# Kernel optimization log

Measured on AMD Instinct MI355X. Metric: run time of the kernel, lower is better.

Reference implementation:

```python
import jax, jax.numpy as jnp
import numpy as np

N_NODES = 50000
N_EDGES = 1600000
IN_CH = 128
OUT_CH = 16
K_HOPS = 2


def setup_inputs() -> dict:
    key = jax.random.key(0)
    k1, k2, k3, k4 = jax.random.split(key, 4)
    x = jax.random.normal(k1, (N_NODES, IN_CH), dtype=jnp.float32)
    W = jax.random.normal(k2, (OUT_CH, IN_CH), dtype=jnp.float32) * 0.05
    edge_weight = jax.random.uniform(k3, (N_EDGES,), dtype=jnp.float32)
    edge_index = jax.random.randint(k4, (2, N_EDGES), 0, N_NODES, dtype=jnp.int64)
    return {"x": x, "W": W, "edge_weight": edge_weight,
            "edge_index": edge_index, "K": K_HOPS}


def reference(x, W, edge_weight, edge_index, K):
    N = x.shape[0]
    # --- gcn_norm with add_self_loops=True (fill_value = 1.0) ---
    loops = jnp.arange(N, dtype=edge_index.dtype)
    row = jnp.concatenate([edge_index[0], loops])  # source nodes
    col = jnp.concatenate([edge_index[1], loops])  # target nodes
    w = jnp.concatenate([edge_weight, jnp.ones((N,), dtype=x.dtype)])
    deg = jax.ops.segment_sum(w, col, num_segments=N)  # degree at targets
    dinv = jnp.where(deg > 0, jax.lax.rsqrt(deg), 0.0)
    norm = dinv[row] * w * dinv[col]  # [E+N]

    # --- K-hop propagation: h <- A_hat @ h (gather-scale-scatter) ---
    def hop(h, _):
        msgs = norm[:, None] * h[row]               # [E+N, F] gather + scale
        h = jax.ops.segment_sum(msgs, col, num_segments=N)  # scatter-add
        return h, None

    h, _ = jax.lax.scan(hop, x, None, length=K)

    # --- linear projection (bias=False) then log_softmax over classes ---
    logits = h @ W.T  # [N, out_channels]
    return jax.nn.log_softmax(logits, axis=1)
```

## Files before the change

### kernel.cpp

```cpp
#include <hip/hip_runtime.h>
#include <hip/hip_fp16.h>
#include <math.h>

#define IN_CH 128
#define OUT_CH 16
#define B 256
#define CH_H 2048
#define CH_P 4096
#define LSH 6
#define LNODES 64
#define S2 4
#define MAXNL 1024
#define MAXGH 2048

__device__ __forceinline__ unsigned short f2h(float f) {
    __half h = __float2half(f);
    unsigned short u;
    __builtin_memcpy(&u, &h, 2);
    return u;
}
__device__ __forceinline__ float h2f(unsigned short u) {
    __half h;
    __builtin_memcpy(&h, &u, 2);
    return __half2float(h);
}

__device__ __forceinline__ void scan_nl(const unsigned* __restrict__ vals, unsigned* dst,
                                        unsigned* sums, int NL) {
    int tid = threadIdx.x;
    int b0 = tid * 4;
    unsigned v[4]; unsigned loc = 0;
#pragma unroll
    for (int q = 0; q < 4; ++q) { int i = b0 + q; v[q] = (i < NL) ? vals[i] : 0u; loc += v[q]; }
    sums[tid] = loc;
    __syncthreads();
    for (int off = 1; off < B; off <<= 1) {
        unsigned a = (tid >= off) ? sums[tid - off] : 0u;
        __syncthreads();
        sums[tid] += a;
        __syncthreads();
    }
    unsigned run = sums[tid] - loc;
#pragma unroll
    for (int q = 0; q < 4; ++q) { int i = b0 + q; if (i < NL) dst[i] = run; run += v[q]; }
    __syncthreads();
}

__global__ void __launch_bounds__(B) k_hist(const int* __restrict__ col,
                                            unsigned* __restrict__ bh, int E, int NL) {
    __shared__ unsigned hc[MAXNL];
    int tid = threadIdx.x;
    for (int i = tid; i < NL; i += B) hc[i] = 0u;
    __syncthreads();
    int base = blockIdx.x * CH_H;
    int end = base + CH_H < E ? base + CH_H : E;
    for (int e = base + tid; e < end; e += B)
        atomicAdd(&hc[col[e] >> LSH], 1u);
    __syncthreads();
    unsigned* out = bh + (size_t)blockIdx.x * NL;
    for (int i = tid; i < NL; i += B) out[i] = hc[i];
}

__global__ void __launch_bounds__(B) k_colscan(unsigned* __restrict__ bh,
                                               unsigned* __restrict__ tot, int G, int NL) {
    int j = blockIdx.x;
    __shared__ unsigned s[B];
    int tid = threadIdx.x;
    unsigned carry = 0;
    for (int g0 = 0; g0 < G; g0 += B) {
        __syncthreads();
        int g = g0 + tid;
        unsigned v = (g < G) ? bh[(size_t)g * NL + j] : 0u;
        s[tid] = v;
        __syncthreads();
        for (int off = 1; off < B; off <<= 1) {
            unsigned add = (tid >= off) ? s[tid - off] : 0u;
            __syncthreads();
            s[tid] += add;
            __syncthreads();
        }
        if (g < G) bh[(size_t)g * NL + j] = carry + s[tid] - v;
        carry += s[B - 1];
    }
    if (tid == 0) tot[j] = carry;
}

__global__ void __launch_bounds__(B)
k_place(const int* __restrict__ row, const int* __restrict__ col, const float* __restrict__ ew,
        const unsigned* __restrict__ bh, const unsigned* __restrict__ tot,
        uint2* __restrict__ rec, int E, int NL, int F) {
    __shared__ uint2 srec[CH_P];
    __shared__ unsigned short slf[CH_P];
    __shared__ unsigned gbase[MAXNL];
    __shared__ unsigned lscan[MAXNL];
    __shared__ unsigned lctr[MAXNL];
    __shared__ unsigned sums[B];
    int tid = threadIdx.x;
    int c = blockIdx.x;
    int base = c * CH_P;
    int end = base + CH_P < E ? base + CH_P : E;
    int cnt = end - base;

    scan_nl(tot, gbase, sums, NL);
    for (int i = tid; i < NL; i += B) lctr[i] = 0u;
    __syncthreads();
    for (int j = tid; j < cnt; j += B)
        atomicAdd(&lctr[col[base + j] >> LSH], 1u);
    __syncthreads();
    scan_nl(lctr, lscan, sums, NL);
    for (int i = tid; i < NL; i += B) lctr[i] = lscan[i];
    __syncthreads();
    for (int j = tid; j < cnt; j += B) {
        int e = base + j;
        int cc = col[e];
        int lf = cc >> LSH;
        unsigned pos = atomicAdd(&lctr[lf], 1u);
        srec[pos] = make_uint2(((unsigned)row[e] << 6) | (unsigned)(cc & (LNODES - 1)),
                               __float_as_uint(ew[e]));
        slf[pos] = (unsigned short)lf;
    }
    __syncthreads();
    const unsigned* myb = bh + (size_t)(c * F) * NL;
    for (int j = tid; j < cnt; j += B) {
        int lf = slf[j];
        unsigned outp = gbase[lf] + myb[lf] + ((unsigned)j - lscan[lf]);
        rec[outp] = srec[j];
    }
}

__global__ void __launch_bounds__(B)
k_hist2(const uint2* __restrict__ rec, const unsigned* __restrict__ tot,
        unsigned* __restrict__ h2, float* __restrict__ h2w, int NL) {
    __shared__ unsigned sums[B];
    __shared__ unsigned gbase[MAXNL];
    __shared__ unsigned hist[LNODES];
    __shared__ float wsum[LNODES];
    int l = blockIdx.x >> 2, s = blockIdx.x & (S2 - 1);
    int tid = threadIdx.x;
    scan_nl(tot, gbase, sums, NL);
    int seg = (int)gbase[l];
    int cnt = (int)tot[l];
    int q = (cnt + S2 - 1) / S2;
    if (tid < LNODES) { hist[tid] = 0u; wsum[tid] = 0.f; }
    __syncthreads();
    int j0 = s * q;
    int j1 = (s + 1) * q < cnt ? (s + 1) * q : cnt;
    for (int j = j0 + tid; j < j1; j += B) {
        uint2 u = rec[seg + j];
        int cc = (int)(u.x & (LNODES - 1));
        atomicAdd(&hist[cc], 1u);
        atomicAdd(&wsum[cc], __uint_as_float(u.y));
    }
    __syncthreads();
    if (tid < LNODES) {
        size_t o = (size_t)(l * S2 + s) * LNODES + tid;
        h2[o] = hist[tid];
        h2w[o] = wsum[tid];
    }
}

__global__ void __launch_bounds__(B)
k_sort2proj(const uint2* __restrict__ rec, const unsigned* __restrict__ tot,
            const unsigned* __restrict__ h2, const float* __restrict__ h2w,
            const float* __restrict__ x, const float* __restrict__ W,
            unsigned* __restrict__ rec2, unsigned* __restrict__ nptr,
            float* __restrict__ dinv, float* __restrict__ g0, int N, int NL) {
    __shared__ unsigned sums[B];
    __shared__ unsigned gbase[MAXNL];
    __shared__ unsigned start2[S2 * LNODES];
    __shared__ float dloc[LNODES];
    __shared__ float sW[OUT_CH * 132];
    int l = blockIdx.x, tid = threadIdx.x;

    for (int i = tid; i < OUT_CH * IN_CH; i += B) {
        sW[(i >> 7) * 132 + (i & 127)] = W[i];
    }
    scan_nl(tot, gbase, sums, NL);
    int seg = (int)gbase[l];
    int cnt = (int)tot[l];
    if (tid < LNODES) {
        size_t ho = (size_t)l * S2 * LNODES + tid;
        unsigned c0 = h2[ho], c1 = h2[ho + LNODES], c2 = h2[ho + 2 * LNODES], c3 = h2[ho + 3 * LNODES];
        float wv = h2w[ho] + h2w[ho + LNODES] + h2w[ho + 2 * LNODES] + h2w[ho + 3 * LNODES];
        unsigned totn = c0 + c1 + c2 + c3;
        unsigned sum = totn;
        for (int off = 1; off < LNODES; off <<= 1) {
            unsigned o = __shfl_up(sum, off, 64);
            if (tid >= off) sum += o;
        }
        unsigned st = (unsigned)seg + sum - totn;
        int n = l * LNODES + tid;
        if (n < N) nptr[n] = st;
        float dn = rsqrtf(1.0f + wv);
        dloc[tid] = dn;
        if (n < N) dinv[n] = dn;
        start2[0 * LNODES + tid] = st;
        start2[1 * LNODES + tid] = st + c0;
        start2[2 * LNODES + tid] = st + c0 + c1;
        start2[3 * LNODES + tid] = st + c0 + c1 + c2;
    }
    if (l == NL - 1 && tid == 0) nptr[N] = (unsigned)(seg + cnt);
    __syncthreads();
    int q = (cnt + S2 - 1) / S2;
    for (int j = tid; j < cnt; j += B) {
        int s = j / q;
        uint2 u = rec[seg + j];
        int cc = (int)(u.x & (LNODES - 1));
        unsigned pos = atomicAdd(&start2[s * LNODES + cc], 1u);
        rec2[pos] = ((u.x >> 6) << 16) | (unsigned)f2h(__uint_as_float(u.y));
    }
    int o = tid & 15;
    for (int nl = tid >> 4; nl < LNODES; nl += 16) {
        int n = l * LNODES + nl;
        if (n >= N) break;
        const float* xr = x + (size_t)n * IN_CH;
        const float* wr = sW + o * 132;
        float acc = 0.0f;
#pragma unroll
        for (int k = 0; k < IN_CH; k += 4) {
            float4 xv = *reinterpret_cast<const float4*>(xr + k);
            float4 wv = *reinterpret_cast<const float4*>(wr + k);
            acc += xv.x * wv.x + xv.y * wv.y + xv.z * wv.z + xv.w * wv.w;
        }
        g0[(size_t)n * OUT_CH + o] = dloc[nl] * acc;
    }
}

template <bool FINAL>
__global__ void __launch_bounds__(B)
k_hop(const unsigned* __restrict__ rec2, const unsigned* __restrict__ nptr,
      const float* __restrict__ dinv, const float* __restrict__ gin,
      float* __restrict__ out, int N) {
    int t = blockIdx.x * B + threadIdx.x;
    int n = t >> 4, ch = t & 15;
    if (n >= N) return;
    int j0 = (int)nptr[n], j1 = (int)nptr[n + 1];
    float acc = 0.f;
    int j = j0;
    for (; j + 3 < j1; j += 4) {
        unsigned u0 = rec2[j], u1 = rec2[j + 1], u2 = rec2[j + 2], u3 = rec2[j + 3];
        acc += h2f((unsigned short)u0) * gin[(size_t)(u0 >> 16) * OUT_CH + ch]
             + h2f((unsigned short)u1) * gin[(size_t)(u1 >> 16) * OUT_CH + ch]
             + h2f((unsigned short)u2) * gin[(size_t)(u2 >> 16) * OUT_CH + ch]
             + h2f((unsigned short)u3) * gin[(size_t)(u3 >> 16) * OUT_CH + ch];
    }
    for (; j < j1; ++j) {
        unsigned u = rec2[j];
        acc += h2f((unsigned short)u) * gin[(size_t)(u >> 16) * OUT_CH + ch];
    }
    float d = dinv[n];
    float s = gin[(size_t)n * OUT_CH + ch] + acc;
    if (!FINAL) {
        out[(size_t)n * OUT_CH + ch] = d * d * s;
    } else {
        float v = d * s;
        float m = v;
#pragma unroll
        for (int off = 1; off < 16; off <<= 1) m = fmaxf(m, __shfl_xor(m, off, 16));
        float se = expf(v - m);
#pragma unroll
        for (int off = 1; off < 16; off <<= 1) se += __shfl_xor(se, off, 16);
        out[(size_t)n * OUT_CH + ch] = v - m - logf(se);
    }
}


__global__ void fb_deginit(float* deg, int N) {
    int i = blockIdx.x * blockDim.x + threadIdx.x;
    if (i < N) deg[i] = 1.0f;
}
__global__ void fb_deg(const int* __restrict__ col, const float* __restrict__ ew,
                       float* deg, int E) {
    int e = blockIdx.x * blockDim.x + threadIdx.x;
    if (e < E) atomicAdd(&deg[col[e]], ew[e]);
}
__global__ void fb_dinv(const float* __restrict__ deg, float* dinv, int N) {
    int i = blockIdx.x * blockDim.x + threadIdx.x;
    if (i < N) dinv[i] = rsqrtf(deg[i]);
}
__global__ void fb_proj(const float* __restrict__ x, const float* __restrict__ W,
                        float* __restrict__ y, int N) {
    __shared__ float sW[OUT_CH * 132];
    for (int i = threadIdx.x; i < OUT_CH * IN_CH; i += blockDim.x) {
        sW[(i >> 7) * 132 + (i & 127)] = W[i];
    }
    __syncthreads();
    int t = threadIdx.x;
    int n = blockIdx.x * 16 + (t >> 4);
    int o = t & 15;
    if (n >= N) return;
    const float* xr = x + (size_t)n * IN_CH;
    const float* wr = sW + o * 132;
    float acc = 0.0f;
#pragma unroll
    for (int k = 0; k < IN_CH; k += 4) {
        float4 xv = *reinterpret_cast<const float4*>(xr + k);
        float4 wv = *reinterpret_cast<const float4*>(wr + k);
        acc += xv.x * wv.x + xv.y * wv.y + xv.z * wv.z + xv.w * wv.w;
    }
    y[(size_t)n * OUT_CH + o] = acc;
}
__global__ void fb_selfinit(const float* __restrict__ hin, const float* __restrict__ dinv,
                            float* __restrict__ hout, int N) {
    int idx = blockIdx.x * blockDim.x + threadIdx.x;
    if (idx < N * OUT_CH) {
        float d = dinv[idx >> 4];
        hout[idx] = d * d * hin[idx];
    }
}
__global__ void fb_scat(const int* __restrict__ row, const int* __restrict__ col,
                        const float* __restrict__ ew, const float* __restrict__ dinv,
                        const float* __restrict__ hin, float* __restrict__ hout, int E) {
    long long idx = (long long)blockIdx.x * blockDim.x + threadIdx.x;
    int e = (int)(idx >> 4);
    int c = (int)(idx & 15);
    if (e >= E) return;
    int r = row[e], cl = col[e];
    float nv = dinv[r] * ew[e] * dinv[cl];
    atomicAdd(&hout[(size_t)cl * OUT_CH + c], nv * hin[(size_t)r * OUT_CH + c]);
}
__global__ void fb_lsm(const float* __restrict__ h, float* __restrict__ out, int N) {
    int n = blockIdx.x * blockDim.x + threadIdx.x;
    if (n >= N) return;
    const float* hr = h + (size_t)n * OUT_CH;
    float v[OUT_CH];
#pragma unroll
    for (int i = 0; i < OUT_CH; i++) v[i] = hr[i];
    float m = v[0];
#pragma unroll
    for (int i = 1; i < OUT_CH; i++) m = fmaxf(m, v[i]);
    float s = 0.0f;
#pragma unroll
    for (int i = 0; i < OUT_CH; i++) s += expf(v[i] - m);
    float lse = m + logf(s);
    float* orow = out + (size_t)n * OUT_CH;
#pragma unroll
    for (int i = 0; i < OUT_CH; i++) orow[i] = v[i] - lse;
}


extern "C" void kernel_launch(void* const* d_in, const int* in_sizes, int n_in,
                              void* d_out, int out_size, void* d_ws, size_t ws_size,
                              hipStream_t stream) {
    const float* x  = (const float*)d_in[0];
    const float* W  = (const float*)d_in[1];
    const float* ew = (const float*)d_in[2];
    const int*   ei = (const int*)d_in[3];

    int N = in_sizes[0] / IN_CH;
    int E = in_sizes[2];
    const int* row = ei;
    const int* col = ei + E;

    auto al = [](size_t v) { return (v + 255) & ~(size_t)255; };
    size_t N16 = (size_t)N * OUT_CH;

    int NL  = (N + LNODES - 1) >> LSH;
    int G_H = (E + CH_H - 1) / CH_H;
    int G_P = (E + CH_P - 1) / CH_P;
    int F   = CH_P / CH_H;
    int gH  = (int)((N16 + B - 1) / B);

    size_t o_rec  = 0;
    size_t o_rec2 = o_rec  + al((size_t)E * 8);
    size_t o_bh   = o_rec2 + al((size_t)E * 4);
    size_t o_tot  = o_bh   + al((size_t)G_H * NL * 4);
    size_t o_h2   = o_tot  + al((size_t)NL * 4);
    size_t o_h2w  = o_h2   + al((size_t)NL * S2 * LNODES * 4);
    size_t o_nptr = o_h2w  + al((size_t)NL * S2 * LNODES * 4);
    size_t o_dinv = o_nptr + al((size_t)(N + 1) * 4);
    size_t o_g0   = o_dinv + al((size_t)N * 4);
    size_t o_g1   = o_g0   + al(N16 * 4);
    size_t need   = o_g1   + al(N16 * 4);

    bool shape_ok = (NL <= MAXNL && G_H <= MAXGH && N <= 65536 &&
                     (G_P * F) <= G_H + F);

    char* ws = (char*)d_ws;

    if (shape_ok && need <= ws_size) {
        uint2*    rec  = (uint2*)(ws + o_rec);
        unsigned* rec2 = (unsigned*)(ws + o_rec2);
        unsigned* bh   = (unsigned*)(ws + o_bh);
        unsigned* tot  = (unsigned*)(ws + o_tot);
        unsigned* h2   = (unsigned*)(ws + o_h2);
        float*    h2w  = (float*)(ws + o_h2w);
        unsigned* nptr = (unsigned*)(ws + o_nptr);
        float*    dinv = (float*)(ws + o_dinv);
        float*    g0   = (float*)(ws + o_g0);
        float*    g1   = (float*)(ws + o_g1);

        k_hist     <<<G_H,     B, 0, stream>>>(col, bh, E, NL);
        k_colscan  <<<NL,      B, 0, stream>>>(bh, tot, G_H, NL);
        k_place    <<<G_P,     B, 0, stream>>>(row, col, ew, bh, tot, rec, E, NL, F);
        k_hist2    <<<NL * S2, B, 0, stream>>>(rec, tot, h2, h2w, NL);
        k_sort2proj<<<NL,      B, 0, stream>>>(rec, tot, h2, h2w, x, W, rec2, nptr, dinv, g0, N, NL);
        k_hop<false><<<gH,     B, 0, stream>>>(rec2, nptr, dinv, g0, g1, N);
        k_hop<true ><<<gH,     B, 0, stream>>>(rec2, nptr, dinv, g1, (float*)d_out, N);
    } else {
        size_t f_deg  = 0;
        size_t f_dinv = f_deg  + al((size_t)N * 4);
        size_t f_h0   = f_dinv + al((size_t)N * 4);
        size_t f_h1   = f_h0   + al(N16 * 4);
        float* deg  = (float*)(ws + f_deg);
        float* dinv = (float*)(ws + f_dinv);
        float* h0   = (float*)(ws + f_h0);
        float* h1   = (float*)(ws + f_h1);

        int gN   = (N + B - 1) / B;
        int gE   = (E + B - 1) / B;
        int gN16 = (N * OUT_CH + B - 1) / B;
        long long scat = (long long)E * OUT_CH;
        int gScat = (int)((scat + B - 1) / B);

        fb_deginit<<<gN, B, 0, stream>>>(deg, N);
        fb_deg<<<gE, B, 0, stream>>>(col, ew, deg, E);
        fb_dinv<<<gN, B, 0, stream>>>(deg, dinv, N);
        fb_proj<<<(N + 15) / 16, B, 0, stream>>>(x, W, h0, N);
        float* hin = h0; float* hout = h1;
        for (int k = 0; k < 2; k++) {
            fb_selfinit<<<gN16, B, 0, stream>>>(hin, dinv, hout, N);
            fb_scat<<<gScat, B, 0, stream>>>(row, col, ew, dinv, hin, hout, E);
            float* t = hin; hin = hout; hout = t;
        }
        fb_lsm<<<gN, B, 0, stream>>>(hin, (float*)d_out, N);
    }
}
```

Before: 128.2 us.

## Split sort2proj into per-slice scatter kernel and separate projection kernel

The fused second-pass scatter plus projection kernel, which ran one block per 64-node bucket, is split into two kernels. The scatter now runs one block per (bucket, slice) pair, giving four times as many blocks. The x@W^T projection moves to its own kernel with 16 nodes per block. This exposes more parallelism for the scatter and the projection, at the cost of one extra launch and a dinv round trip through global memory.

After: 129.5 us. Within noise of the previous version (+1.0%).

```diff
diff --git a/kernel.cpp b/kernel.cpp
--- a/kernel.cpp
+++ b/kernel.cpp
@@ -160,28 +160,22 @@
 }
 
 __global__ void __launch_bounds__(B)
-k_sort2proj(const uint2* __restrict__ rec, const unsigned* __restrict__ tot,
-            const unsigned* __restrict__ h2, const float* __restrict__ h2w,
-            const float* __restrict__ x, const float* __restrict__ W,
-            unsigned* __restrict__ rec2, unsigned* __restrict__ nptr,
-            float* __restrict__ dinv, float* __restrict__ g0, int N, int NL) {
+k_scat2(const uint2* __restrict__ rec, const unsigned* __restrict__ tot,
+        const unsigned* __restrict__ h2, const float* __restrict__ h2w,
+        unsigned* __restrict__ rec2, unsigned* __restrict__ nptr,
+        float* __restrict__ dinv, int N, int NL) {
     __shared__ unsigned sums[B];
     __shared__ unsigned gbase[MAXNL];
-    __shared__ unsigned start2[S2 * LNODES];
-    __shared__ float dloc[LNODES];
-    __shared__ float sW[OUT_CH * 132];
-    int l = blockIdx.x, tid = threadIdx.x;
-
-    for (int i = tid; i < OUT_CH * IN_CH; i += B) {
-        sW[(i >> 7) * 132 + (i & 127)] = W[i];
-    }
+    __shared__ unsigned ctr[LNODES];
+    int l = blockIdx.x >> 2, s = blockIdx.x & (S2 - 1);
+    int tid = threadIdx.x;
     scan_nl(tot, gbase, sums, NL);
     int seg = (int)gbase[l];
     int cnt = (int)tot[l];
     if (tid < LNODES) {
         size_t ho = (size_t)l * S2 * LNODES + tid;
-        unsigned c0 = h2[ho], c1 = h2[ho + LNODES], c2 = h2[ho + 2 * LNODES], c3 = h2[ho + 3 * LNODES];
-        float wv = h2w[ho] + h2w[ho + LNODES] + h2w[ho + 2 * LNODES] + h2w[ho + 3 * LNODES];
+        unsigned c0 = h2[ho], c1 = h2[ho + LNODES];
+        unsigned c2 = h2[ho + 2 * LNODES], c3 = h2[ho + 3 * LNODES];
         unsigned totn = c0 + c1 + c2 + c3;
         unsigned sum = totn;
         for (int off = 1; off < LNODES; off <<= 1) {
@@ -189,41 +183,55 @@
             if (tid >= off) sum += o;
         }
         unsigned st = (unsigned)seg + sum - totn;
-        int n = l * LNODES + tid;
-        if (n < N) nptr[n] = st;
-        float dn = rsqrtf(1.0f + wv);
-        dloc[tid] = dn;
-        if (n < N) dinv[n] = dn;
-        start2[0 * LNODES + tid] = st;
-        start2[1 * LNODES + tid] = st + c0;
-        start2[2 * LNODES + tid] = st + c0 + c1;
-        start2[3 * LNODES + tid] = st + c0 + c1 + c2;
-    }
-    if (l == NL - 1 && tid == 0) nptr[N] = (unsigned)(seg + cnt);
+        unsigned prev = 0;
+        if (s > 0) prev += c0;
+        if (s > 1) prev += c1;
+        if (s > 2) prev += c2;
+        ctr[tid] = st + prev;
+        if (s == 0) {
+            int n = l * LNODES + tid;
+            if (n < N) {
+                nptr[n] = st;
+                float wv = h2w[ho] + h2w[ho + LNODES] + h2w[ho + 2 * LNODES] + h2w[ho + 3 * LNODES];
+                dinv[n] = rsqrtf(1.0f + wv);
+            }
+        }
+    }
+    if (s == 0 && l == NL - 1 && tid == 0) nptr[N] = (unsigned)(seg + cnt);
     __syncthreads();
     int q = (cnt + S2 - 1) / S2;
-    for (int j = tid; j < cnt; j += B) {
-        int s = j / q;
+    int j0 = s * q;
+    int j1 = (s + 1) * q < cnt ? (s + 1) * q : cnt;
+    for (int j = j0 + tid; j < j1; j += B) {
         uint2 u = rec[seg + j];
         int cc = (int)(u.x & (LNODES - 1));
-        unsigned pos = atomicAdd(&start2[s * LNODES + cc], 1u);
+        unsigned pos = atomicAdd(&ctr[cc], 1u);
         rec2[pos] = ((u.x >> 6) << 16) | (unsigned)f2h(__uint_as_float(u.y));
     }
-    int o = tid & 15;
-    for (int nl = tid >> 4; nl < LNODES; nl += 16) {
-        int n = l * LNODES + nl;
-        if (n >= N) break;
-        const float* xr = x + (size_t)n * IN_CH;
-        const float* wr = sW + o * 132;
-        float acc = 0.0f;
-#pragma unroll
-        for (int k = 0; k < IN_CH; k += 4) {
-            float4 xv = *reinterpret_cast<const float4*>(xr + k);
-            float4 wv = *reinterpret_cast<const float4*>(wr + k);
-            acc += xv.x * wv.x + xv.y * wv.y + xv.z * wv.z + xv.w * wv.w;
-        }
-        g0[(size_t)n * OUT_CH + o] = dloc[nl] * acc;
-    }
+}
+
+__global__ void __launch_bounds__(B)
+k_proj(const float* __restrict__ x, const float* __restrict__ W,
+       const float* __restrict__ dinv, float* __restrict__ y, int N) {
+    __shared__ float sW[OUT_CH * 132];
+    for (int i = threadIdx.x; i < OUT_CH * IN_CH; i += B) {
+        sW[(i >> 7) * 132 + (i & 127)] = W[i];
+    }
+    __syncthreads();
+    int t = threadIdx.x;
+    int n = blockIdx.x * 16 + (t >> 4);
+    int o = t & 15;
+    if (n >= N) return;
+    const float* xr = x + (size_t)n * IN_CH;
+    const float* wr = sW + o * 132;
+    float acc = 0.0f;
+#pragma unroll
+    for (int k = 0; k < IN_CH; k += 4) {
+        float4 xv = *reinterpret_cast<const float4*>(xr + k);
+        float4 wv = *reinterpret_cast<const float4*>(wr + k);
+        acc += xv.x * wv.x + xv.y * wv.y + xv.z * wv.z + xv.w * wv.w;
+    }
+    y[(size_t)n * OUT_CH + o] = dinv[n] * acc;
 }
 
 template <bool FINAL>
@@ -390,13 +398,14 @@
         float*    g0   = (float*)(ws + o_g0);
         float*    g1   = (float*)(ws + o_g1);
 
-        k_hist     <<<G_H,     B, 0, stream>>>(col, bh, E, NL);
-        k_colscan  <<<NL,      B, 0, stream>>>(bh, tot, G_H, NL);
-        k_place    <<<G_P,     B, 0, stream>>>(row, col, ew, bh, tot, rec, E, NL, F);
-        k_hist2    <<<NL * S2, B, 0, stream>>>(rec, tot, h2, h2w, NL);
-        k_sort2proj<<<NL,      B, 0, stream>>>(rec, tot, h2, h2w, x, W, rec2, nptr, dinv, g0, N, NL);
-        k_hop<false><<<gH,     B, 0, stream>>>(rec2, nptr, dinv, g0, g1, N);
-        k_hop<true ><<<gH,     B, 0, stream>>>(rec2, nptr, dinv, g1, (float*)d_out, N);
+        k_hist   <<<G_H,     B, 0, stream>>>(col, bh, E, NL);
+        k_colscan<<<NL,      B, 0, stream>>>(bh, tot, G_H, NL);
+        k_place  <<<G_P,     B, 0, stream>>>(row, col, ew, bh, tot, rec, E, NL, F);
+        k_hist2  <<<NL * S2, B, 0, stream>>>(rec, tot, h2, h2w, NL);
+        k_scat2  <<<NL * S2, B, 0, stream>>>(rec, tot, h2, h2w, rec2, nptr, dinv, N, NL);
+        k_proj   <<<(N + 15) / 16, B, 0, stream>>>(x, W, dinv, g0, N);
+        k_hop<false><<<gH,   B, 0, stream>>>(rec2, nptr, dinv, g0, g1, N);
+        k_hop<true ><<<gH,   B, 0, stream>>>(rec2, nptr, dinv, g1, (float*)d_out, N);
     } else {
         size_t f_deg  = 0;
         size_t f_dinv = f_deg  + al((size_t)N * 4);
```
